# Kernel tuning notes

Hardware: AMD Instinct MI355X
Metric: run time of the kernel (lower is better)

The kernel has to match this reference:

```python
import jax, jax.numpy as jnp
import numpy as np

B, E, S, D = 32, 64, 50, 300   # batch, sentences/essay, words/sentence, word dim
F = 100                        # conv filters (cnn_lstm_convunits_size)
H = 100                        # lstm units (cnn_lstm_att_pool_size)
W_WIN = 5                      # word window length


def setup_inputs() -> dict:
    key = jax.random.key(0)
    ks = jax.random.split(key, 12)
    n = lambda k, shape: (jax.random.normal(k, shape, jnp.float32) * 0.05)
    return {
        "essays": jax.random.normal(ks[0], (B, E, S, D), jnp.float32),
        "conv_k": n(ks[1], (1, W_WIN, D, F)),      # HWIO
        "conv_b": jnp.zeros((F,), jnp.float32),
        "att1_mat": n(ks[2], (F, F)),
        "att1_bias": n(ks[3], (F,)),
        "att1_vec": n(ks[4], (F, 1)),
        "lstm_W": n(ks[5], (F + H, 4 * H)),        # TF BasicLSTMCell kernel, gate order i,j,f,o
        "lstm_b": jnp.zeros((4 * H,), jnp.float32),
        "att2_mat": n(ks[6], (H, H)),
        "att2_bias": n(ks[7], (H,)),
        "att2_vec": n(ks[8], (H, 1)),
        "dense_w": n(ks[9], (H, 1)),
        "dense_b": jnp.zeros((1,), jnp.float32),
    }


def reference(essays, conv_k, conv_b, att1_mat, att1_bias, att1_vec,
              lstm_W, lstm_b, att2_mat, att2_bias, att2_vec,
              dense_w, dense_b):
    # conv2d, kernel [1, w_window_len], SAME padding, relu  -> [B,E,S,F]
    conv1 = jax.lax.conv_general_dilated(
        essays, conv_k, window_strides=(1, 1), padding="SAME",
        dimension_numbers=("NHWC", "HWIO", "NHWC"))
    conv1 = jax.nn.relu(conv1 + conv_b)

    # attention pooling over words (axis=2)
    a1 = jnp.tanh(jnp.einsum("besf,fg->besg", conv1, att1_mat) + att1_bias)
    a1 = jnp.einsum("besg,go->beso", a1, att1_vec)          # [B,E,S,1]
    a1 = jax.nn.softmax(a1, axis=2)
    sent = jnp.sum(a1 * conv1, axis=2)                       # [B,E,F]

    # BasicLSTMCell (forget_bias=1.0, gate order i,j,f,o) over sentence axis
    hdim = lstm_b.shape[0] // 4
    bsz = essays.shape[0]

    def step(carry, xt):
        c, h = carry
        z = jnp.concatenate([xt, h], axis=1) @ lstm_W + lstm_b
        i, j, f, o = jnp.split(z, 4, axis=1)
        c = c * jax.nn.sigmoid(f + 1.0) + jax.nn.sigmoid(i) * jnp.tanh(j)
        h = jax.nn.sigmoid(o) * jnp.tanh(c)
        return (c, h), h

    init = (jnp.zeros((bsz, hdim), sent.dtype), jnp.zeros((bsz, hdim), sent.dtype))
    xs = jnp.swapaxes(sent, 0, 1)                            # [E,B,F]
    _, hs = jax.lax.scan(step, init, xs)
    lstm = jnp.swapaxes(hs, 0, 1)                            # [B,E,H]

    # attention pooling over sentences (axis=1)
    a2 = jnp.tanh(jnp.einsum("beh,hg->beg", lstm, att2_mat) + att2_bias)
    a2 = jnp.einsum("beg,go->beo", a2, att2_vec)             # [B,E,1]
    a2 = jax.nn.softmax(a2, axis=1)
    essay_repr = jnp.sum(a2 * lstm, axis=1)                  # [B,H]

    preds = jax.nn.sigmoid(essay_repr @ dense_w + dense_b).reshape(-1)  # [B]
    return preds
```

## Files before the change

kernel.cpp:

```cpp
#include <hip/hip_runtime.h>
#include <hip/hip_bf16.h>
#include <stdint.h>

#define Bsz 32
#define Esz 64
#define Ssz 50
#define Dsz 300
#define Fsz 100
#define Hsz 100
#define WWIN 5

#define PX   328
#define PC   136
#define KT_CONV 50
#define NTILES  7
#define MTILES  4
#define NGRP 2214

typedef __attribute__((ext_vector_type(8))) short bf16x8;
typedef __attribute__((ext_vector_type(8))) unsigned short u16x8;
typedef __attribute__((ext_vector_type(4))) float f32x4;

__device__ __forceinline__ float sigmoid_fast(float x) {
    return 1.0f / (1.0f + __expf(-x));
}
__device__ __forceinline__ float tanhf_fast(float x) {
    const float ax = fabsf(x);
    const float e = __expf(2.0f * ax);
    const float t = 1.0f - 2.0f / (e + 1.0f);
    return copysignf(t, x);
}

__device__ __forceinline__ unsigned short f2bf(float x) {
    union { __hip_bfloat16 h; unsigned short u; } cv;
    cv.h = __float2bfloat16(x);
    return cv.u;
}
__device__ __forceinline__ unsigned int f2bf2(float lo, float hi) {
    union { __hip_bfloat162 h2; unsigned int u; } cv;
    cv.h2 = __float22bfloat162_rn(make_float2(lo, hi));
    return cv.u;
}
__device__ __forceinline__ float bf2f(unsigned short b) {
    union { uint32_t u; float f; } v; v.u = ((uint32_t)b) << 16;
    return v.f;
}

#define N_BTGC (KT_CONV * 112 * 32)
#define N_BTGA (4 * 112 * 32)
#define N_BTGW (4 * 400 * 32)

__global__ __launch_bounds__(256) void prep_kernel(
    const float* __restrict__ conv_k, const float* __restrict__ att1_mat,
    const float* __restrict__ lstm_W,
    unsigned short* __restrict__ BtgC, unsigned short* __restrict__ BtgA,
    unsigned short* __restrict__ BtgW)
{
    const int total = N_BTGC + N_BTGA + N_BTGW;
    for (int i = blockIdx.x * 256 + threadIdx.x; i < total; i += gridDim.x * 256) {
        if (i < N_BTGC) {
            const int kt = i / (112 * 32);
            const int r  = i % (112 * 32);
            const int n  = r / 32;
            const int kk = r % 32;
            const int w  = kt / 10;
            const int d  = (kt % 10) * 32 + kk;
            float val = (d < Dsz && n < Fsz) ? conv_k[((size_t)w * Dsz + d) * Fsz + n] : 0.f;
            BtgC[i] = f2bf(val);
        } else if (i < N_BTGC + N_BTGA) {
            const int j  = i - N_BTGC;
            const int kt = j / (112 * 32);
            const int r  = j % (112 * 32);
            const int n  = r / 32;
            const int kk = r % 32;
            const int k  = kt * 32 + kk;
            float val = (k < Fsz && n < Fsz) ? att1_mat[(size_t)k * Fsz + n] : 0.f;
            BtgA[j] = f2bf(val);
        } else {
            const int j  = i - N_BTGC - N_BTGA;
            const int kt = j / (400 * 32);
            const int r  = j % (400 * 32);
            const int n  = r / 32;
            const int kk = r % 32;
            const int k  = kt * 32 + kk;
            float val = (k < Fsz) ? lstm_W[(size_t)k * 400 + n] : 0.f;
            BtgW[j] = f2bf(val);
        }
    }
}

template<int G>
__device__ __forceinline__ void conv_loadB(
    const unsigned short* __restrict__ BtgC, int boff0, int boff1, bool has1,
    bf16x8 (&bR)[5][2])
{
#pragma unroll
    for (int i = 0; i < 5; ++i) {
        const int kt = G * 5 + i;
        bR[i][0] = *reinterpret_cast<const bf16x8*>(BtgC + kt * 3584 + boff0);
        bR[i][1] = has1 ? *reinterpret_cast<const bf16x8*>(BtgC + kt * 3584 + boff1)
                        : (bf16x8)0;
    }
}

template<int G>
__device__ __forceinline__ void conv_compute(
    const unsigned short* buf, const int (&abase)[MTILES], bool has1,
    const bf16x8 (&bR)[5][2], f32x4 (&acc)[MTILES][2])
{
#pragma unroll
    for (int i = 0; i < 5; ++i) {
        const int kt  = G * 5 + i;
        const int w   = kt / 10;
        const int t   = kt % 10;
        const int off = w * PX + t * 32;
#pragma unroll
        for (int mt = 0; mt < MTILES; ++mt) {
            const bf16x8 af = *reinterpret_cast<const bf16x8*>(&buf[abase[mt] + off]);
            acc[mt][0] = __builtin_amdgcn_mfma_f32_16x16x32_bf16(af, bR[i][0], acc[mt][0], 0, 0, 0);
            if (has1)
                acc[mt][1] = __builtin_amdgcn_mfma_f32_16x16x32_bf16(af, bR[i][1], acc[mt][1], 0, 0, 0);
        }
    }
}

__global__ __launch_bounds__(256, 3) void conv_att1_kernel(
    const float* __restrict__ essays,
    const unsigned short* __restrict__ BtgC,
    const unsigned short* __restrict__ BtgA,
    const float* __restrict__ conv_b,
    const float* __restrict__ att1_bias,
    const float* __restrict__ att1_vec,
    unsigned short* __restrict__ sent_bf)
{
    __shared__ __align__(16) unsigned short buf[54 * PX];
    __shared__ float u_s[64];
    __shared__ float alpha_s[64];

    const int be  = blockIdx.x;
    const int tid = threadIdx.x;
    const int lane = tid & 63;
    const int wid  = tid >> 6;
    const int ln   = lane & 15;
    const int qd   = lane >> 4;
    const float* in_g = essays + (size_t)be * (Ssz * Dsz);

    if (tid < 64) u_s[tid] = 0.f;

    {
        float4 va[9], vb[9];
        int rr[9], cc[9];
        bool hv[9], fv[9], gv[9];
#pragma unroll
        for (int it = 0; it < 9; ++it) {
            const int g  = tid + it * 256;
            const int r  = g / 41;
            const int c8 = (g - r * 41) * 8;
            const int s  = r - 2;
            gv[it] = (g < NGRP);
            hv[it] = gv[it] && (s >= 0) && (s < Ssz) && (c8 < Dsz);
            fv[it] = hv[it] && (c8 + 8 <= Dsz);
            const float* base = in_g + (hv[it] ? (s * Dsz + c8) : 0);
            va[it] = *reinterpret_cast<const float4*>(base);
            vb[it] = *reinterpret_cast<const float4*>(fv[it] ? base + 4 : base);
            rr[it] = r; cc[it] = c8;
        }
#pragma unroll
        for (int it = 0; it < 9; ++it) {
            if (!gv[it]) continue;
            const float e0 = hv[it] ? va[it].x : 0.f;
            const float e1 = hv[it] ? va[it].y : 0.f;
            const float e2 = hv[it] ? va[it].z : 0.f;
            const float e3 = hv[it] ? va[it].w : 0.f;
            const float e4 = fv[it] ? vb[it].x : 0.f;
            const float e5 = fv[it] ? vb[it].y : 0.f;
            const float e6 = fv[it] ? vb[it].z : 0.f;
            const float e7 = fv[it] ? vb[it].w : 0.f;
            uint4 o;
            o.x = f2bf2(e0, e1);
            o.y = f2bf2(e2, e3);
            o.z = f2bf2(e4, e5);
            o.w = f2bf2(e6, e7);
            *reinterpret_cast<uint4*>(&buf[rr[it] * PX + cc[it]]) = o;
        }
    }
    __syncthreads();

    const int nt0 = wid;
    const int nt1 = wid + 4;
    const bool has1 = (nt1 < NTILES);
    const int boff0 = (nt0 * 16 + ln) * 32 + 8 * qd;
    const int boff1 = (nt1 * 16 + ln) * 32 + 8 * qd;

    int abase[MTILES];
#pragma unroll
    for (int mt = 0; mt < MTILES; ++mt) {
        const int m = mt * 16 + ln;
        abase[mt] = (m < Ssz ? m : Ssz - 1) * PX + 8 * qd;
    }

    f32x4 acc[MTILES][2];
#pragma unroll
    for (int mt = 0; mt < MTILES; ++mt) { acc[mt][0] = (f32x4)0.f; acc[mt][1] = (f32x4)0.f; }

    {
        bf16x8 bX[5][2], bY[5][2];
        conv_loadB<0>(BtgC, boff0, boff1, has1, bX);
        conv_loadB<1>(BtgC, boff0, boff1, has1, bY);
        conv_compute<0>(buf, abase, has1, bX, acc);
        conv_loadB<2>(BtgC, boff0, boff1, has1, bX);
        conv_compute<1>(buf, abase, has1, bY, acc);
        conv_loadB<3>(BtgC, boff0, boff1, has1, bY);
        conv_compute<2>(buf, abase, has1, bX, acc);
        conv_loadB<4>(BtgC, boff0, boff1, has1, bX);
        conv_compute<3>(buf, abase, has1, bY, acc);
        conv_loadB<5>(BtgC, boff0, boff1, has1, bY);
        conv_compute<4>(buf, abase, has1, bX, acc);
        conv_loadB<6>(BtgC, boff0, boff1, has1, bX);
        conv_compute<5>(buf, abase, has1, bY, acc);
        conv_loadB<7>(BtgC, boff0, boff1, has1, bY);
        conv_compute<6>(buf, abase, has1, bX, acc);
        conv_loadB<8>(BtgC, boff0, boff1, has1, bX);
        conv_compute<7>(buf, abase, has1, bY, acc);
        conv_loadB<9>(BtgC, boff0, boff1, has1, bY);
        conv_compute<8>(buf, abase, has1, bX, acc);
        conv_compute<9>(buf, abase, has1, bY, acc);
    }

    bf16x8 a1b[4][2];
#pragma unroll
    for (int kt = 0; kt < 4; ++kt) {
        a1b[kt][0] = *reinterpret_cast<const bf16x8*>(BtgA + kt * 3584 + boff0);
        a1b[kt][1] = has1 ? *reinterpret_cast<const bf16x8*>(BtgA + kt * 3584 + boff1)
                          : (bf16x8)0;
    }
    __syncthreads();

#pragma unroll
    for (int nl = 0; nl < 2; ++nl) {
        const int nt = (nl == 0) ? nt0 : nt1;
        if (nl == 1 && !has1) break;
        const int n_g = nt * 16 + ln;
        const float bias = (n_g < Fsz) ? conv_b[n_g] : 0.f;
#pragma unroll
        for (int mt = 0; mt < MTILES; ++mt) {
#pragma unroll
            for (int j = 0; j < 4; ++j) {
                const int m_row = mt * 16 + qd * 4 + j;
                const float v = fmaxf(acc[mt][nl][j] + bias, 0.f);
                buf[m_row * PC + n_g] = f2bf(v);
            }
        }
    }
    for (int idx = tid; idx < 64 * 2; idx += 256) {
        const int row = idx >> 1;
        const int c = 112 + (idx & 1) * 8;
        *reinterpret_cast<u16x8*>(&buf[row * PC + c]) = (u16x8)0;
    }
    __syncthreads();

    f32x4 acc2[MTILES][2];
#pragma unroll
    for (int mt = 0; mt < MTILES; ++mt) { acc2[mt][0] = (f32x4)0.f; acc2[mt][1] = (f32x4)0.f; }

#pragma unroll
    for (int kt = 0; kt < 4; ++kt) {
        bf16x8 afrag[MTILES];
#pragma unroll
        for (int mt = 0; mt < MTILES; ++mt) {
            afrag[mt] = *reinterpret_cast<const bf16x8*>(
                &buf[(mt * 16 + ln) * PC + kt * 32 + 8 * qd]);
        }
#pragma unroll
        for (int mt = 0; mt < MTILES; ++mt) {
            acc2[mt][0] = __builtin_amdgcn_mfma_f32_16x16x32_bf16(afrag[mt], a1b[kt][0], acc2[mt][0], 0, 0, 0);
            if (has1)
                acc2[mt][1] = __builtin_amdgcn_mfma_f32_16x16x32_bf16(afrag[mt], a1b[kt][1], acc2[mt][1], 0, 0, 0);
        }
    }

    {
        const int g0 = nt0 * 16 + ln;
        const float b1v0 = att1_bias[g0];
        const float vv0  = att1_vec[g0];
        const int g1 = nt1 * 16 + ln;
        const bool g1v = has1 && (g1 < Fsz);
        const float b1v1 = g1v ? att1_bias[g1] : 0.f;
        const float vv1  = g1v ? att1_vec[g1]  : 0.f;
#pragma unroll
        for (int mt = 0; mt < MTILES; ++mt) {
#pragma unroll
            for (int j = 0; j < 4; ++j) {
                const int m_row = mt * 16 + qd * 4 + j;
                float val = 0.f;
                if (m_row < Ssz) {
                    val = tanhf_fast(acc2[mt][0][j] + b1v0) * vv0;
                    if (g1v) val += tanhf_fast(acc2[mt][1][j] + b1v1) * vv1;
                }
                val += __shfl_xor(val, 1);
                val += __shfl_xor(val, 2);
                val += __shfl_xor(val, 4);
                val += __shfl_xor(val, 8);
                if (ln == 0 && m_row < Ssz) atomicAdd(&u_s[m_row], val);
            }
        }
    }
    __syncthreads();

    if (tid < 64) {
        const float uv = (tid < Ssz) ? u_s[tid] : -1e30f;
        float m = uv;
#pragma unroll
        for (int off = 32; off > 0; off >>= 1) m = fmaxf(m, __shfl_xor(m, off));
        float e = (tid < Ssz) ? __expf(uv - m) : 0.f;
        float sum = e;
#pragma unroll
        for (int off = 32; off > 0; off >>= 1) sum += __shfl_xor(sum, off);
        alpha_s[tid] = e / sum;
    }
    __syncthreads();

    if (tid < 128) {
        unsigned short v = 0;
        if (tid < Fsz) {
            float a = 0.f;
            for (int s = 0; s < Ssz; ++s) a += alpha_s[s] * bf2f(buf[s * PC + tid]);
            v = f2bf(a);
        }
        sent_bf[(size_t)be * 128 + tid] = v;
    }
}

__global__ __launch_bounds__(256) void xpart_kernel(
    const unsigned short* __restrict__ sent_bf,
    const unsigned short* __restrict__ BtgW,
    const float* __restrict__ lstm_b,
    float* __restrict__ xpart)
{
    const int wid  = threadIdx.x >> 6;
    const int mt   = blockIdx.x * 4 + wid;
    const int lane = threadIdx.x & 63;
    const int ln   = lane & 15;
    const int qd   = lane >> 4;
    const int m0   = mt * 16;

    f32x4 acc[25];
#pragma unroll
    for (int nt = 0; nt < 25; ++nt) acc[nt] = (f32x4)0.f;

#pragma unroll
    for (int kt = 0; kt < 4; ++kt) {
        const bf16x8 a = *reinterpret_cast<const bf16x8*>(
            sent_bf + (size_t)(m0 + ln) * 128 + kt * 32 + 8 * qd);
#pragma unroll
        for (int nt = 0; nt < 25; ++nt) {
            const bf16x8 b = *reinterpret_cast<const bf16x8*>(
                BtgW + ((size_t)kt * 400 + nt * 16 + ln) * 32 + 8 * qd);
            acc[nt] = __builtin_amdgcn_mfma_f32_16x16x32_bf16(a, b, acc[nt], 0, 0, 0);
        }
    }

#pragma unroll
    for (int nt = 0; nt < 25; ++nt) {
        const int col = nt * 16 + ln;
        const float bias = lstm_b[col];
#pragma unroll
        for (int j = 0; j < 4; ++j) {
            const int row = m0 + qd * 4 + j;
            xpart[(size_t)row * 400 + col] = acc[nt][j] + bias;
        }
    }
}

__global__ __launch_bounds__(448) void lstm_att2_kernel(
    const float* __restrict__ xpart,
    const float* __restrict__ lstm_W,
    const float* __restrict__ att2_mat,
    const float* __restrict__ att2_bias,
    const float* __restrict__ att2_vec,
    const float* __restrict__ dense_w,
    const float* __restrict__ dense_b,
    float* __restrict__ out)
{
    __shared__ __align__(16) float h_s[Hsz];
    __shared__ float z_s[400];
    __shared__ __align__(16) float hist[Esz][Hsz];
    __shared__ float w2_s[Esz * Hsz];
    __shared__ float u2_s[Esz];
    __shared__ float alpha2_s[Esz];
    __shared__ float repr_s[Hsz];

    const int b = blockIdx.x;
    const int tid = threadIdx.x;
    const bool actv = tid < 400;

    float w[100];
    if (actv) {
#pragma unroll
        for (int k = 0; k < 100; ++k) w[k] = lstm_W[(size_t)(Fsz + k) * 400 + tid];
    }
    float c = 0.f;
    if (tid < Hsz) h_s[tid] = 0.f;
    __syncthreads();

    float xp_cur = actv ? xpart[(size_t)b * Esz * 400 + tid] : 0.f;
    const float4* h4 = reinterpret_cast<const float4*>(h_s);

    for (int t = 0; t < Esz; ++t) {
        const float xp_next = (actv && (t + 1) < Esz)
            ? xpart[((size_t)b * Esz + t + 1) * 400 + tid] : 0.f;
        if (actv) {
            float z0 = xp_cur, z1 = 0.f, z2 = 0.f, z3 = 0.f;
#pragma unroll
            for (int k4 = 0; k4 < 25; ++k4) {
                const float4 hv = h4[k4];
                z0 += hv.x * w[4 * k4 + 0];
                z1 += hv.y * w[4 * k4 + 1];
                z2 += hv.z * w[4 * k4 + 2];
                z3 += hv.w * w[4 * k4 + 3];
            }
            z_s[tid] = (z0 + z1) + (z2 + z3);
        }
        __syncthreads();

        if (tid < Hsz) {
            const float zi = z_s[tid];
            const float zj = z_s[tid + 100];
            const float zf = z_s[tid + 200];
            const float zo = z_s[tid + 300];
            c = c * sigmoid_fast(zf + 1.0f) + sigmoid_fast(zi) * tanhf_fast(zj);
            const float h = sigmoid_fast(zo) * tanhf_fast(c);
            h_s[tid] = h;
            hist[t][tid] = h;
        }
        __syncthreads();
        xp_cur = xp_next;
    }

    for (int idx = tid; idx < Esz * Hsz; idx += 448) {
        const int e = idx / Hsz;
        const int g = idx - e * Hsz;
        const float* lp = hist[e];
        float a0 = 0.f, a1 = 0.f, a2 = 0.f, a3 = 0.f;
        for (int k = 0; k < Hsz; k += 4) {
            a0 += lp[k + 0] * att2_mat[(k + 0) * Hsz + g];
            a1 += lp[k + 1] * att2_mat[(k + 1) * Hsz + g];
            a2 += lp[k + 2] * att2_mat[(k + 2) * Hsz + g];
            a3 += lp[k + 3] * att2_mat[(k + 3) * Hsz + g];
        }
        w2_s[idx] = tanhf_fast(att2_bias[g] + ((a0 + a1) + (a2 + a3))) * att2_vec[g];
    }
    __syncthreads();

    if (tid < Esz) {
        float acc = 0.f;
        const float* wp = w2_s + tid * Hsz;
        for (int g = 0; g < Hsz; ++g) acc += wp[g];
        u2_s[tid] = acc;
    }
    __syncthreads();

    if (tid < 64) {
        const float uv = u2_s[tid];
        float m = uv;
#pragma unroll
        for (int off = 32; off > 0; off >>= 1) m = fmaxf(m, __shfl_xor(m, off));
        float e = __expf(uv - m);
        float sum = e;
#pragma unroll
        for (int off = 32; off > 0; off >>= 1) sum += __shfl_xor(sum, off);
        alpha2_s[tid] = e / sum;
    }
    __syncthreads();

    if (tid < Hsz) {
        float acc = 0.f;
        for (int e = 0; e < Esz; ++e) acc += alpha2_s[e] * hist[e][tid];
        repr_s[tid] = acc;
    }
    __syncthreads();

    if (tid == 0) {
        float acc = dense_b[0];
        for (int hh = 0; hh < Hsz; ++hh) acc += repr_s[hh] * dense_w[hh];
        out[b] = sigmoid_fast(acc);
    }
}

extern "C" void kernel_launch(void* const* d_in, const int* in_sizes, int n_in,
                              void* d_out, int out_size, void* d_ws, size_t ws_size,
                              hipStream_t stream) {
    const float* essays    = (const float*)d_in[0];
    const float* conv_k    = (const float*)d_in[1];
    const float* conv_b    = (const float*)d_in[2];
    const float* att1_mat  = (const float*)d_in[3];
    const float* att1_bias = (const float*)d_in[4];
    const float* att1_vec  = (const float*)d_in[5];
    const float* lstm_W    = (const float*)d_in[6];
    const float* lstm_b    = (const float*)d_in[7];
    const float* att2_mat  = (const float*)d_in[8];
    const float* att2_bias = (const float*)d_in[9];
    const float* att2_vec  = (const float*)d_in[10];
    const float* dense_w   = (const float*)d_in[11];
    const float* dense_b   = (const float*)d_in[12];

    float* out = (float*)d_out;

    char* ws = (char*)d_ws;
    unsigned short* sent_bf = (unsigned short*)ws;
    float* xpart = (float*)(ws + 524288);
    unsigned short* BtgC = (unsigned short*)(ws + 3801088);
    unsigned short* BtgA = (unsigned short*)(ws + 4159488);
    unsigned short* BtgW = (unsigned short*)(ws + 4188160);

    prep_kernel<<<512, 256, 0, stream>>>(conv_k, att1_mat, lstm_W, BtgC, BtgA, BtgW);
    conv_att1_kernel<<<Bsz * Esz, 256, 0, stream>>>(
        essays, BtgC, BtgA, conv_b, att1_bias, att1_vec, sent_bf);
    xpart_kernel<<<32, 256, 0, stream>>>(sent_bf, BtgW, lstm_b, xpart);
    lstm_att2_kernel<<<Bsz, 448, 0, stream>>>(
        xpart, lstm_W, att2_mat, att2_bias, att2_vec, dense_w, dense_b, out);
}
```

Measured before the change: 211.6 us.

## Process two essays-sentences per conv block to reuse conv weight fragments

Each conv_att1 block now handles two (batch, sentence) items with a doubled shared buffer and doubled accumulators, so each loaded conv/attention weight fragment feeds twice as many MFMAs. The grid is halved and launch bounds drop to 2 blocks per SM. This cuts global weight-load traffic per item and amortises per-block overhead, but it raises register and LDS pressure and reduces occupancy.

```diff
diff --git a/kernel.cpp b/kernel.cpp
--- a/kernel.cpp
+++ b/kernel.cpp
@@ -105,8 +105,9 @@
 
 template<int G>
 __device__ __forceinline__ void conv_compute(
-    const unsigned short* buf, const int (&abase)[MTILES], bool has1,
-    const bf16x8 (&bR)[5][2], f32x4 (&acc)[MTILES][2])
+    const unsigned short* buf0, const unsigned short* buf1,
+    const int (&abase)[MTILES], bool has1,
+    const bf16x8 (&bR)[5][2], f32x4 (&acc)[2][MTILES][2])
 {
 #pragma unroll
     for (int i = 0; i < 5; ++i) {
@@ -116,15 +117,19 @@
         const int off = w * PX + t * 32;
 #pragma unroll
         for (int mt = 0; mt < MTILES; ++mt) {
-            const bf16x8 af = *reinterpret_cast<const bf16x8*>(&buf[abase[mt] + off]);
-            acc[mt][0] = __builtin_amdgcn_mfma_f32_16x16x32_bf16(af, bR[i][0], acc[mt][0], 0, 0, 0);
-            if (has1)
-                acc[mt][1] = __builtin_amdgcn_mfma_f32_16x16x32_bf16(af, bR[i][1], acc[mt][1], 0, 0, 0);
-        }
-    }
-}
-
-__global__ __launch_bounds__(256, 3) void conv_att1_kernel(
+            const bf16x8 af0 = *reinterpret_cast<const bf16x8*>(&buf0[abase[mt] + off]);
+            const bf16x8 af1 = *reinterpret_cast<const bf16x8*>(&buf1[abase[mt] + off]);
+            acc[0][mt][0] = __builtin_amdgcn_mfma_f32_16x16x32_bf16(af0, bR[i][0], acc[0][mt][0], 0, 0, 0);
+            acc[1][mt][0] = __builtin_amdgcn_mfma_f32_16x16x32_bf16(af1, bR[i][0], acc[1][mt][0], 0, 0, 0);
+            if (has1) {
+                acc[0][mt][1] = __builtin_amdgcn_mfma_f32_16x16x32_bf16(af0, bR[i][1], acc[0][mt][1], 0, 0, 0);
+                acc[1][mt][1] = __builtin_amdgcn_mfma_f32_16x16x32_bf16(af1, bR[i][1], acc[1][mt][1], 0, 0, 0);
+            }
+        }
+    }
+}
+
+__global__ __launch_bounds__(256, 2) void conv_att1_kernel(
     const float* __restrict__ essays,
     const unsigned short* __restrict__ BtgC,
     const unsigned short* __restrict__ BtgA,
@@ -133,21 +138,22 @@
     const float* __restrict__ att1_vec,
     unsigned short* __restrict__ sent_bf)
 {
-    __shared__ __align__(16) unsigned short buf[54 * PX];
-    __shared__ float u_s[64];
-    __shared__ float alpha_s[64];
-
-    const int be  = blockIdx.x;
+    __shared__ __align__(16) unsigned short buf[2][54 * PX];
+    __shared__ float u_s[2][64];
+    __shared__ float alpha_s[2][64];
+
+    const int be0 = blockIdx.x * 2;
     const int tid = threadIdx.x;
     const int lane = tid & 63;
     const int wid  = tid >> 6;
     const int ln   = lane & 15;
     const int qd   = lane >> 4;
-    const float* in_g = essays + (size_t)be * (Ssz * Dsz);
-
-    if (tid < 64) u_s[tid] = 0.f;
-
-    {
+
+    if (tid < 128) u_s[tid >> 6][tid & 63] = 0.f;
+
+#pragma unroll
+    for (int es = 0; es < 2; ++es) {
+        const float* in_g = essays + (size_t)(be0 + es) * (Ssz * Dsz);
         float4 va[9], vb[9];
         int rr[9], cc[9];
         bool hv[9], fv[9], gv[9];
@@ -181,7 +187,7 @@
             o.y = f2bf2(e2, e3);
             o.z = f2bf2(e4, e5);
             o.w = f2bf2(e6, e7);
-            *reinterpret_cast<uint4*>(&buf[rr[it] * PX + cc[it]]) = o;
+            *reinterpret_cast<uint4*>(&buf[es][rr[it] * PX + cc[it]]) = o;
         }
     }
     __syncthreads();
@@ -199,32 +205,36 @@
         abase[mt] = (m < Ssz ? m : Ssz - 1) * PX + 8 * qd;
     }
 
-    f32x4 acc[MTILES][2];
-#pragma unroll
-    for (int mt = 0; mt < MTILES; ++mt) { acc[mt][0] = (f32x4)0.f; acc[mt][1] = (f32x4)0.f; }
+    f32x4 acc[2][MTILES][2];
+#pragma unroll
+    for (int es = 0; es < 2; ++es)
+#pragma unroll
+        for (int mt = 0; mt < MTILES; ++mt) { acc[es][mt][0] = (f32x4)0.f; acc[es][mt][1] = (f32x4)0.f; }
 
     {
+        const unsigned short* b0p = buf[0];
+        const unsigned short* b1p = buf[1];
         bf16x8 bX[5][2], bY[5][2];
         conv_loadB<0>(BtgC, boff0, boff1, has1, bX);
         conv_loadB<1>(BtgC, boff0, boff1, has1, bY);
-        conv_compute<0>(buf, abase, has1, bX, acc);
+        conv_compute<0>(b0p, b1p, abase, has1, bX, acc);
         conv_loadB<2>(BtgC, boff0, boff1, has1, bX);
-        conv_compute<1>(buf, abase, has1, bY, acc);
+        conv_compute<1>(b0p, b1p, abase, has1, bY, acc);
         conv_loadB<3>(BtgC, boff0, boff1, has1, bY);
-        conv_compute<2>(buf, abase, has1, bX, acc);
+        conv_compute<2>(b0p, b1p, abase, has1, bX, acc);
         conv_loadB<4>(BtgC, boff0, boff1, has1, bX);
-        conv_compute<3>(buf, abase, has1, bY, acc);
+        conv_compute<3>(b0p, b1p, abase, has1, bY, acc);
         conv_loadB<5>(BtgC, boff0, boff1, has1, bY);
-        conv_compute<4>(buf, abase, has1, bX, acc);
+        conv_compute<4>(b0p, b1p, abase, has1, bX, acc);
         conv_loadB<6>(BtgC, boff0, boff1, has1, bX);
-        conv_compute<5>(buf, abase, has1, bY, acc);
+        conv_compute<5>(b0p, b1p, abase, has1, bY, acc);
         conv_loadB<7>(BtgC, boff0, boff1, has1, bY);
-        conv_compute<6>(buf, abase, has1, bX, acc);
+        conv_compute<6>(b0p, b1p, abase, has1, bX, acc);
         conv_loadB<8>(BtgC, boff0, boff1, has1, bX);
-        conv_compute<7>(buf, abase, has1, bY, acc);
+        conv_compute<7>(b0p, b1p, abase, has1, bY, acc);
         conv_loadB<9>(BtgC, boff0, boff1, has1, bY);
-        conv_compute<8>(buf, abase, has1, bX, acc);
-        conv_compute<9>(buf, abase, has1, bY, acc);
+        conv_compute<8>(b0p, b1p, abase, has1, bX, acc);
+        conv_compute<9>(b0p, b1p, abase, has1, bY, acc);
     }
 
     bf16x8 a1b[4][2];
@@ -236,46 +246,52 @@
     }
     __syncthreads();
 
-#pragma unroll
-    for (int nl = 0; nl < 2; ++nl) {
-        const int nt = (nl == 0) ? nt0 : nt1;
-        if (nl == 1 && !has1) break;
-        const int n_g = nt * 16 + ln;
-        const float bias = (n_g < Fsz) ? conv_b[n_g] : 0.f;
-#pragma unroll
-        for (int mt = 0; mt < MTILES; ++mt) {
-#pragma unroll
-            for (int j = 0; j < 4; ++j) {
-                const int m_row = mt * 16 + qd * 4 + j;
-                const float v = fmaxf(acc[mt][nl][j] + bias, 0.f);
-                buf[m_row * PC + n_g] = f2bf(v);
+    {
+        const float bias0 = conv_b[nt0 * 16 + ln];
+        const int n_g1 = nt1 * 16 + ln;
+        const bool g1ok = has1 && (n_g1 < Fsz);
+        const float bias1 = g1ok ? conv_b[n_g1] : 0.f;
+#pragma unroll
+        for (int es = 0; es < 2; ++es) {
+#pragma unroll
+            for (int mt = 0; mt < MTILES; ++mt) {
+#pragma unroll
+                for (int j = 0; j < 4; ++j) {
+                    const int m_row = mt * 16 + qd * 4 + j;
+                    buf[es][m_row * PC + nt0 * 16 + ln] = f2bf(fmaxf(acc[es][mt][0][j] + bias0, 0.f));
+                    if (g1ok)
+                        buf[es][m_row * PC + n_g1] = f2bf(fmaxf(acc[es][mt][1][j] + bias1, 0.f));
+                }
             }
         }
     }
-    for (int idx = tid; idx < 64 * 2; idx += 256) {
-        const int row = idx >> 1;
-        const int c = 112 + (idx & 1) * 8;
-        *reinterpret_cast<u16x8*>(&buf[row * PC + c]) = (u16x8)0;
-    }
-    __syncthreads();
-
-    f32x4 acc2[MTILES][2];
-#pragma unroll
-    for (int mt = 0; mt < MTILES; ++mt) { acc2[mt][0] = (f32x4)0.f; acc2[mt][1] = (f32x4)0.f; }
+    for (int idx = tid; idx < 2 * 64 * 2; idx += 256) {
+        const int es = idx >> 7;
+        const int r2 = idx & 127;
+        const int row = r2 >> 1;
+        const int c = 112 + (r2 & 1) * 8;
+        *reinterpret_cast<u16x8*>(&buf[es][row * PC + c]) = (u16x8)0;
+    }
+    __syncthreads();
+
+    f32x4 acc2[2][MTILES][2];
+#pragma unroll
+    for (int es = 0; es < 2; ++es)
+#pragma unroll
+        for (int mt = 0; mt < MTILES; ++mt) { acc2[es][mt][0] = (f32x4)0.f; acc2[es][mt][1] = (f32x4)0.f; }
 
 #pragma unroll
     for (int kt = 0; kt < 4; ++kt) {
-        bf16x8 afrag[MTILES];
-#pragma unroll
-        for (int mt = 0; mt < MTILES; ++mt) {
-            afrag[mt] = *reinterpret_cast<const bf16x8*>(
-                &buf[(mt * 16 + ln) * PC + kt * 32 + 8 * qd]);
-        }
-#pragma unroll
-        for (int mt = 0; mt < MTILES; ++mt) {
-            acc2[mt][0] = __builtin_amdgcn_mfma_f32_16x16x32_bf16(afrag[mt], a1b[kt][0], acc2[mt][0], 0, 0, 0);
-            if (has1)
-                acc2[mt][1] = __builtin_amdgcn_mfma_f32_16x16x32_bf16(afrag[mt], a1b[kt][1], acc2[mt][1], 0, 0, 0);
+#pragma unroll
+        for (int es = 0; es < 2; ++es) {
+#pragma unroll
+            for (int mt = 0; mt < MTILES; ++mt) {
+                const bf16x8 af = *reinterpret_cast<const bf16x8*>(
+                    &buf[es][(mt * 16 + ln) * PC + kt * 32 + 8 * qd]);
+                acc2[es][mt][0] = __builtin_amdgcn_mfma_f32_16x16x32_bf16(af, a1b[kt][0], acc2[es][mt][0], 0, 0, 0);
+                if (has1)
+                    acc2[es][mt][1] = __builtin_amdgcn_mfma_f32_16x16x32_bf16(af, a1b[kt][1], acc2[es][mt][1], 0, 0, 0);
+            }
         }
     }
 
@@ -288,46 +304,51 @@
         const float b1v1 = g1v ? att1_bias[g1] : 0.f;
         const float vv1  = g1v ? att1_vec[g1]  : 0.f;
 #pragma unroll
-        for (int mt = 0; mt < MTILES; ++mt) {
-#pragma unroll
-            for (int j = 0; j < 4; ++j) {
-                const int m_row = mt * 16 + qd * 4 + j;
-                float val = 0.f;
-                if (m_row < Ssz) {
-                    val = tanhf_fast(acc2[mt][0][j] + b1v0) * vv0;
-                    if (g1v) val += tanhf_fast(acc2[mt][1][j] + b1v1) * vv1;
+        for (int es = 0; es < 2; ++es) {
+#pragma unroll
+            for (int mt = 0; mt < MTILES; ++mt) {
+#pragma unroll
+                for (int j = 0; j < 4; ++j) {
+                    const int m_row = mt * 16 + qd * 4 + j;
+                    float val = 0.f;
+                    if (m_row < Ssz) {
+                        val = tanhf_fast(acc2[es][mt][0][j] + b1v0) * vv0;
+                        if (g1v) val += tanhf_fast(acc2[es][mt][1][j] + b1v1) * vv1;
+                    }
+                    val += __shfl_xor(val, 1);
+                    val += __shfl_xor(val, 2);
+                    val += __shfl_xor(val, 4);
+                    val += __shfl_xor(val, 8);
+                    if (ln == 0 && m_row < Ssz) atomicAdd(&u_s[es][m_row], val);
                 }
-                val += __shfl_xor(val, 1);
-                val += __shfl_xor(val, 2);
-                val += __shfl_xor(val, 4);
-                val += __shfl_xor(val, 8);
-                if (ln == 0 && m_row < Ssz) atomicAdd(&u_s[m_row], val);
             }
         }
     }
     __syncthreads();
 
-    if (tid < 64) {
-        const float uv = (tid < Ssz) ? u_s[tid] : -1e30f;
+    if (wid < 2) {
+        const float uv = (lane < Ssz) ? u_s[wid][lane] : -1e30f;
         float m = uv;
 #pragma unroll
         for (int off = 32; off > 0; off >>= 1) m = fmaxf(m, __shfl_xor(m, off));
-        float e = (tid < Ssz) ? __expf(uv - m) : 0.f;
+        float e = (lane < Ssz) ? __expf(uv - m) : 0.f;
         float sum = e;
 #pragma unroll
         for (int off = 32; off > 0; off >>= 1) sum += __shfl_xor(sum, off);
-        alpha_s[tid] = e / sum;
-    }
-    __syncthreads();
-
-    if (tid < 128) {
+        alpha_s[wid][lane] = e / sum;
+    }
+    __syncthreads();
+
+    {
+        const int es = tid >> 7;
+        const int f  = tid & 127;
         unsigned short v = 0;
-        if (tid < Fsz) {
+        if (f < Fsz) {
             float a = 0.f;
-            for (int s = 0; s < Ssz; ++s) a += alpha_s[s] * bf2f(buf[s * PC + tid]);
+            for (int s = 0; s < Ssz; ++s) a += alpha_s[es][s] * bf2f(buf[es][s * PC + f]);
             v = f2bf(a);
         }
-        sent_bf[(size_t)be * 128 + tid] = v;
+        sent_bf[(size_t)(be0 + es) * 128 + f] = v;
     }
 }
 
@@ -514,7 +535,7 @@
     unsigned short* BtgW = (unsigned short*)(ws + 4188160);
 
     prep_kernel<<<512, 256, 0, stream>>>(conv_k, att1_mat, lstm_W, BtgC, BtgA, BtgW);
-    conv_att1_kernel<<<Bsz * Esz, 256, 0, stream>>>(
+    conv_att1_kernel<<<Bsz * Esz / 2, 256, 0, stream>>>(
         essays, BtgC, BtgA, conv_b, att1_bias, att1_vec, sent_bf);
     xpart_kernel<<<32, 256, 0, stream>>>(sent_bf, BtgW, lstm_b, xpart);
     lstm_att2_kernel<<<Bsz, 448, 0, stream>>>(
```

After: 208.9 us. Within noise of the previous version (-1.3%).
